# Optimization experiments

Measured on AMD Instinct MI355X. Metric: run time of the kernel, lower is better.

The kernel has to match this reference:

```python
import jax, jax.numpy as jnp
import numpy as np

BSZ, SEQLEN, D = 32, 256, 128


def setup_inputs() -> dict:
    key = jax.random.key(0)
    # Near-identity init (I + eps*N) keeps the length-256 matrix product
    # numerically stable, as in standard CMOW embeddings.
    noise = jax.random.normal(key, (BSZ, SEQLEN, D, D), dtype=jnp.float32)
    input_embeds = jnp.eye(D, dtype=jnp.float32) + 0.02 * noise
    return {"input_embeds": input_embeds}


def reference(input_embeds):
    # Cumulative (left-to-right) matrix product along the sequence axis.
    # result[:, i] = E_0 @ E_1 @ ... @ E_i  -- matmul is associative, so we
    # use a log-depth parallel scan instead of a serial per-step bmm loop.
    all_outputs = jax.lax.associative_scan(jnp.matmul, input_embeds, axis=1)
    x = all_outputs[:, -1]  # [bsz, d, d]
    return (x, all_outputs)
```

## Files before the change

### kernel.cpp

```cpp
#include <hip/hip_runtime.h>

typedef _Float16 half8_t __attribute__((ext_vector_type(8)));
typedef _Float16 half4_t __attribute__((ext_vector_type(4)));
typedef float    f32x4   __attribute__((ext_vector_type(4)));

#define BSZ 32
#define SEQ 256
#define DD  128
#define MAT 16384
#define NCH 16
#define CL  16

__device__ __forceinline__ int sw_chunk(int m, int kb) { return (m << 4) + (kb ^ (m & 7)); }
__device__ __forceinline__ int sw_off(int m, int k)    { return (sw_chunk(m, k >> 3) << 3) + (k & 7); }

__device__ __forceinline__ void mm128(const _Float16* __restrict__ Ads,
                                      const _Float16* __restrict__ Bds,
                                      f32x4 acc[4][4],
                                      int qr, int qc, int quad, int l16) {
#pragma unroll
  for (int ks = 0; ks < 4; ++ks) {
    const int kb = ks * 4 + quad;
    half8_t a[4], b[4];
#pragma unroll
    for (int tr = 0; tr < 4; ++tr)
      a[tr] = *(const half8_t*)&Ads[sw_chunk(qr * 64 + tr * 16 + l16, kb) << 3];
#pragma unroll
    for (int tc = 0; tc < 4; ++tc)
      b[tc] = *(const half8_t*)&Bds[sw_chunk(qc * 64 + tc * 16 + l16, kb) << 3];
#pragma unroll
    for (int tr = 0; tr < 4; ++tr)
#pragma unroll
      for (int tc = 0; tc < 4; ++tc)
        acc[tr][tc] = __builtin_amdgcn_mfma_f32_16x16x32_f16(a[tr], b[tc], acc[tr][tc], 0, 0, 0);
  }
}

__device__ __forceinline__ void stage_f16(const _Float16* __restrict__ src,
                                          _Float16* dst, int tid) {
#pragma unroll
  for (int it = 0; it < 8; ++it) {
    int idx = tid + it * 256;
    int m = idx >> 4, kb = idx & 15;
    *(uint4*)&dst[sw_chunk(m, kb) << 3] = ((const uint4*)src)[idx];
  }
}

__device__ __forceinline__ void acc_to_lds(_Float16* Ads, const f32x4 acc[4][4],
                                           int qr, int qc, int quad, int l16) {
#pragma unroll
  for (int tr = 0; tr < 4; ++tr)
#pragma unroll
    for (int tc = 0; tc < 4; ++tc) {
      int m0 = qr * 64 + tr * 16 + quad * 4;
      int n  = qc * 64 + tc * 16 + l16;
#pragma unroll
      for (int r = 0; r < 4; ++r) Ads[sw_off(m0 + r, n)] = (_Float16)acc[tr][tc][r];
    }
}

__device__ __forceinline__ _Float16* pT_slot(float* out_all, int b, int t) {
  return (_Float16*)(out_all + (size_t)(b * SEQ + t) * MAT) + MAT;
}

__global__ __launch_bounds__(256) void k_phase1(const float* __restrict__ in,
                                                float* __restrict__ out_all,
                                                _Float16* __restrict__ Sbuf) {
  __shared__ __align__(16) _Float16 Ads[MAT];
  __shared__ __align__(16) _Float16 Bds[MAT];
  const int tid = threadIdx.x;
  const int b = blockIdx.x >> 4, c = blockIdx.x & 15;
  const int t0 = c * CL;
  const int wave = tid >> 6, lane = tid & 63;
  const int qr = wave >> 1, qc = wave & 1, quad = lane >> 4, l16 = lane & 15;

  {
    const f32x4* src = (const f32x4*)(in + (size_t)(b * SEQ + t0) * MAT);
#pragma unroll
    for (int it = 0; it < 16; ++it) {
      int g = tid + it * 256;
      f32x4 v = src[g];
      int e0 = g << 2, m = e0 >> 7, k0 = e0 & 127;
      half4_t hv;
      hv[0] = (_Float16)v[0]; hv[1] = (_Float16)v[1];
      hv[2] = (_Float16)v[2]; hv[3] = (_Float16)v[3];
      *(half4_t*)&Ads[(sw_chunk(m, k0 >> 3) << 3) + (k0 & 7)] = hv;
    }
  }
  __syncthreads();
  {
    _Float16* dst = pT_slot(out_all, b, t0);
#pragma unroll
    for (int it = 0; it < 8; ++it) {
      int idx = tid + it * 256;
      int n = idx >> 4, m0 = (idx & 15) << 3;
      half8_t v;
#pragma unroll
      for (int j = 0; j < 8; ++j) v[j] = Ads[sw_off(m0 + j, n)];
      *(half8_t*)&dst[n * DD + m0] = v;
    }
  }

  f32x4 acc[4][4];
  for (int i = 1; i < CL; ++i) {
    {
      const f32x4* src = (const f32x4*)(in + (size_t)(b * SEQ + t0 + i) * MAT);
#pragma unroll
      for (int it = 0; it < 16; ++it) {
        int g = tid + it * 256;
        f32x4 v = src[g];
        int e0 = g << 2, k = e0 >> 7, n0 = e0 & 127;
        Bds[sw_off(n0 + 0, k)] = (_Float16)v[0];
        Bds[sw_off(n0 + 1, k)] = (_Float16)v[1];
        Bds[sw_off(n0 + 2, k)] = (_Float16)v[2];
        Bds[sw_off(n0 + 3, k)] = (_Float16)v[3];
      }
    }
    if (i > 1) acc_to_lds(Ads, acc, qr, qc, quad, l16);
    __syncthreads();
#pragma unroll
    for (int tr = 0; tr < 4; ++tr)
#pragma unroll
      for (int tc = 0; tc < 4; ++tc) { f32x4 z = {0.f, 0.f, 0.f, 0.f}; acc[tr][tc] = z; }
    mm128(Ads, Bds, acc, qr, qc, quad, l16);
    {
      _Float16* dst = pT_slot(out_all, b, t0 + i);
#pragma unroll
      for (int tr = 0; tr < 4; ++tr)
#pragma unroll
        for (int tc = 0; tc < 4; ++tc) {
          int m0 = qr * 64 + tr * 16 + quad * 4;
          int n  = qc * 64 + tc * 16 + l16;
          half4_t hv;
          hv[0] = (_Float16)acc[tr][tc][0]; hv[1] = (_Float16)acc[tr][tc][1];
          hv[2] = (_Float16)acc[tr][tc][2]; hv[3] = (_Float16)acc[tr][tc][3];
          *(half4_t*)&dst[n * DD + m0] = hv;
        }
    }
    __syncthreads();
  }

  if (c == 0) {
    acc_to_lds(Ads, acc, qr, qc, quad, l16);
    __syncthreads();
    _Float16* dst = Sbuf + (size_t)b * NCH * MAT;
#pragma unroll
    for (int it = 0; it < 8; ++it) {
      int idx = tid + it * 256;
      int m = idx >> 4, kb = idx & 15;
      *(uint4*)&dst[idx << 3] = *(const uint4*)&Ads[sw_chunk(m, kb) << 3];
    }
  }
}

__global__ __launch_bounds__(256) void k_phase2(const float* __restrict__ out_all,
                                                _Float16* __restrict__ Sbuf,
                                                float* __restrict__ out_x) {
  __shared__ __align__(16) _Float16 Ads[MAT];
  __shared__ __align__(16) _Float16 Bds[MAT];
  const int tid = threadIdx.x, b = blockIdx.x;
  const int wave = tid >> 6, lane = tid & 63;
  const int qr = wave >> 1, qc = wave & 1, quad = lane >> 4, l16 = lane & 15;

  stage_f16(Sbuf + (size_t)b * NCH * MAT, Ads, tid);

  f32x4 acc[4][4];
  for (int cc = 1; cc < NCH; ++cc) {
    stage_f16((const _Float16*)(out_all + (size_t)(b * SEQ + cc * CL + CL - 1) * MAT) + MAT,
              Bds, tid);
    __syncthreads();
#pragma unroll
    for (int tr = 0; tr < 4; ++tr)
#pragma unroll
      for (int tc = 0; tc < 4; ++tc) { f32x4 z = {0.f, 0.f, 0.f, 0.f}; acc[tr][tc] = z; }
    mm128(Ads, Bds, acc, qr, qc, quad, l16);
    __syncthreads();
    if (cc < NCH - 1) {
      acc_to_lds(Ads, acc, qr, qc, quad, l16);
      __syncthreads();
      _Float16* dst = Sbuf + ((size_t)b * NCH + cc) * MAT;
#pragma unroll
      for (int it = 0; it < 8; ++it) {
        int idx = tid + it * 256;
        int m = idx >> 4, kb = idx & 15;
        *(uint4*)&dst[idx << 3] = *(const uint4*)&Ads[sw_chunk(m, kb) << 3];
      }
    } else {
      float* xo = out_x + (size_t)b * MAT;
#pragma unroll
      for (int tr = 0; tr < 4; ++tr)
#pragma unroll
        for (int tc = 0; tc < 4; ++tc) {
          int m0 = qr * 64 + tr * 16 + quad * 4;
          int n  = qc * 64 + tc * 16 + l16;
#pragma unroll
          for (int r = 0; r < 4; ++r) xo[(m0 + r) * DD + n] = acc[tr][tc][r];
        }
    }
  }
}

__global__ __launch_bounds__(256) void k_phase3(float* __restrict__ out_all,
                                                const _Float16* __restrict__ Sbuf) {
  __shared__ __align__(16) _Float16 Ads[MAT];
  __shared__ __align__(16) _Float16 Bds[MAT];
  const int tid = threadIdx.x;
  const int b = blockIdx.x >> 4, c = blockIdx.x & 15;
  const int wave = tid >> 6, lane = tid & 63;
  const int qr = wave >> 1, qc = wave & 1, quad = lane >> 4, l16 = lane & 15;

  if (c == 0) {
    uint4 z; z.x = z.y = z.z = z.w = 0u;
#pragma unroll
    for (int it = 0; it < 8; ++it) *(uint4*)&Ads[(tid + it * 256) << 3] = z;
    __syncthreads();
    if (tid < DD) Ads[sw_off(tid, tid)] = (_Float16)1.0f;
  } else {
    stage_f16(Sbuf + ((size_t)b * NCH + (c - 1)) * MAT, Ads, tid);
  }

  f32x4 acc[4][4];
  for (int i = 0; i < CL; ++i) {
    const int t = c * CL + i;
    float* slot = out_all + (size_t)(b * SEQ + t) * MAT;
    stage_f16((const _Float16*)slot + MAT, Bds, tid);
    __syncthreads();
#pragma unroll
    for (int tr = 0; tr < 4; ++tr)
#pragma unroll
      for (int tc = 0; tc < 4; ++tc) { f32x4 z = {0.f, 0.f, 0.f, 0.f}; acc[tr][tc] = z; }
    mm128(Ads, Bds, acc, qr, qc, quad, l16);
#pragma unroll
    for (int tr = 0; tr < 4; ++tr)
#pragma unroll
      for (int tc = 0; tc < 4; ++tc) {
        int m0 = qr * 64 + tr * 16 + quad * 4;
        int n  = qc * 64 + tc * 16 + l16;
#pragma unroll
        for (int r = 0; r < 4; ++r) slot[(m0 + r) * DD + n] = acc[tr][tc][r];
      }
    __syncthreads();
  }
}

extern "C" void kernel_launch(void* const* d_in, const int* in_sizes, int n_in,
                              void* d_out, int out_size, void* d_ws, size_t ws_size,
                              hipStream_t stream) {
  const float* in = (const float*)d_in[0];
  float* out_x   = (float*)d_out;
  float* out_all = out_x + (size_t)BSZ * MAT;
  _Float16* Sbuf = (_Float16*)d_ws;

  k_phase1<<<dim3(BSZ * NCH), dim3(256), 0, stream>>>(in, out_all, Sbuf);
  k_phase2<<<dim3(BSZ), dim3(256), 0, stream>>>((const float*)out_all, Sbuf, out_x);
  k_phase3<<<dim3(BSZ * NCH), dim3(256), 0, stream>>>(out_all, Sbuf);
}
```

Before: 1.234 ms.

## Reverse operand roles to compute transposed products with prefetched register staging

The three phases now build transposed products (new matrix times the running product held in LDS), so the running accumulator can be written straight back into the B buffer and no longer needs an LDS transpose or a separate Sbuf copy pass. The next step's global data is loaded into registers while the current step computes, and lighter barriers replace __syncthreads. The fp32 outputs are now written as vector stores in transposed order, and launch bounds request two blocks per CU. In exchange, register pressure is higher, and correctness depends on the reversed-operand transposition being consistent across all three phases.

```diff
diff --git a/kernel.cpp b/kernel.cpp
--- a/kernel.cpp
+++ b/kernel.cpp
@@ -14,6 +14,17 @@
 __device__ __forceinline__ int sw_chunk(int m, int kb) { return (m << 4) + (kb ^ (m & 7)); }
 __device__ __forceinline__ int sw_off(int m, int k)    { return (sw_chunk(m, k >> 3) << 3) + (k & 7); }
 
+__device__ __forceinline__ void barrier_lgkm() {
+  asm volatile("s_waitcnt lgkmcnt(0)" ::: "memory");
+  __builtin_amdgcn_s_barrier();
+  asm volatile("" ::: "memory");
+}
+__device__ __forceinline__ void barrier_only() {
+  asm volatile("" ::: "memory");
+  __builtin_amdgcn_s_barrier();
+  asm volatile("" ::: "memory");
+}
+
 __device__ __forceinline__ void mm128(const _Float16* __restrict__ Ads,
                                       const _Float16* __restrict__ Bds,
                                       f32x4 acc[4][4],
@@ -36,36 +47,102 @@
   }
 }
 
-__device__ __forceinline__ void stage_f16(const _Float16* __restrict__ src,
-                                          _Float16* dst, int tid) {
-#pragma unroll
-  for (int it = 0; it < 8; ++it) {
-    int idx = tid + it * 256;
-    int m = idx >> 4, kb = idx & 15;
-    *(uint4*)&dst[sw_chunk(m, kb) << 3] = ((const uint4*)src)[idx];
-  }
-}
-
-__device__ __forceinline__ void acc_to_lds(_Float16* Ads, const f32x4 acc[4][4],
-                                           int qr, int qc, int quad, int l16) {
+__device__ __forceinline__ void tl_f32(const float* __restrict__ src, f32x4 ra[16],
+                                       int colg, int rowg0) {
+#pragma unroll
+  for (int p = 0; p < 4; ++p)
+#pragma unroll
+    for (int j = 0; j < 4; ++j)
+      ra[p * 4 + j] = *(const f32x4*)&src[(((rowg0 + p * 8) << 2) + j) * DD + (colg << 2)];
+}
+__device__ __forceinline__ void tw_f32(_Float16* Ads, const f32x4 ra[16],
+                                       int colg, int rowg0) {
+#pragma unroll
+  for (int p = 0; p < 4; ++p) {
+    const int k0 = (rowg0 + p * 8) << 2;
+    const int kb = k0 >> 3, kpar = k0 & 7;
+#pragma unroll
+    for (int jj = 0; jj < 4; ++jj) {
+      const int n = (colg << 2) + jj;
+      half4_t hv;
+      hv[0] = (_Float16)ra[p * 4 + 0][jj];
+      hv[1] = (_Float16)ra[p * 4 + 1][jj];
+      hv[2] = (_Float16)ra[p * 4 + 2][jj];
+      hv[3] = (_Float16)ra[p * 4 + 3][jj];
+      *(half4_t*)&Ads[(sw_chunk(n, kb) << 3) + kpar] = hv;
+    }
+  }
+}
+
+__device__ __forceinline__ void tl_f16(const _Float16* __restrict__ src, half8_t rp[8],
+                                       int colg, int rowg) {
+#pragma unroll
+  for (int h = 0; h < 2; ++h)
+#pragma unroll
+    for (int j = 0; j < 4; ++j)
+      rp[h * 4 + j] = *(const half8_t*)&src[(((rowg + h * 16) << 2) + j) * DD + (colg << 3)];
+}
+__device__ __forceinline__ void tw_f16(_Float16* Ads, const half8_t rp[8],
+                                       int colg, int rowg) {
+#pragma unroll
+  for (int h = 0; h < 2; ++h) {
+    const int k0 = (rowg + h * 16) << 2;
+    const int kb = k0 >> 3, kpar = k0 & 7;
+#pragma unroll
+    for (int jj = 0; jj < 8; ++jj) {
+      const int n = (colg << 3) + jj;
+      half4_t hv;
+      hv[0] = rp[h * 4 + 0][jj]; hv[1] = rp[h * 4 + 1][jj];
+      hv[2] = rp[h * 4 + 2][jj]; hv[3] = rp[h * 4 + 3][jj];
+      *(half4_t*)&Ads[(sw_chunk(n, kb) << 3) + kpar] = hv;
+    }
+  }
+}
+
+__device__ __forceinline__ void acc_store_f16(_Float16* __restrict__ dst,
+                                              const f32x4 acc[4][4],
+                                              int qr, int qc, int quad, int l16) {
 #pragma unroll
   for (int tr = 0; tr < 4; ++tr)
 #pragma unroll
     for (int tc = 0; tc < 4; ++tc) {
       int m0 = qr * 64 + tr * 16 + quad * 4;
       int n  = qc * 64 + tc * 16 + l16;
-#pragma unroll
-      for (int r = 0; r < 4; ++r) Ads[sw_off(m0 + r, n)] = (_Float16)acc[tr][tc][r];
-    }
-}
-
-__device__ __forceinline__ _Float16* pT_slot(float* out_all, int b, int t) {
+      half4_t hv;
+      hv[0] = (_Float16)acc[tr][tc][0]; hv[1] = (_Float16)acc[tr][tc][1];
+      hv[2] = (_Float16)acc[tr][tc][2]; hv[3] = (_Float16)acc[tr][tc][3];
+      *(half4_t*)&dst[n * DD + m0] = hv;
+    }
+}
+__device__ __forceinline__ void acc_to_bds(_Float16* Bds, const f32x4 acc[4][4],
+                                           int qr, int qc, int quad, int l16) {
+#pragma unroll
+  for (int tr = 0; tr < 4; ++tr)
+#pragma unroll
+    for (int tc = 0; tc < 4; ++tc) {
+      int m0 = qr * 64 + tr * 16 + quad * 4;
+      int n  = qc * 64 + tc * 16 + l16;
+      half4_t hv;
+      hv[0] = (_Float16)acc[tr][tc][0]; hv[1] = (_Float16)acc[tr][tc][1];
+      hv[2] = (_Float16)acc[tr][tc][2]; hv[3] = (_Float16)acc[tr][tc][3];
+      *(half4_t*)&Bds[(sw_chunk(n, m0 >> 3) << 3) + (m0 & 7)] = hv;
+    }
+}
+
+#define ZERO_ACC(acc)                                             \
+  _Pragma("unroll") for (int tr = 0; tr < 4; ++tr)                \
+  _Pragma("unroll") for (int tc = 0; tc < 4; ++tc) {              \
+    f32x4 z = {0.f, 0.f, 0.f, 0.f}; acc[tr][tc] = z; }
+
+__device__ __forceinline__ _Float16* p_slot(float* out_all, int b, int t) {
   return (_Float16*)(out_all + (size_t)(b * SEQ + t) * MAT) + MAT;
 }
-
-__global__ __launch_bounds__(256) void k_phase1(const float* __restrict__ in,
-                                                float* __restrict__ out_all,
-                                                _Float16* __restrict__ Sbuf) {
+__device__ __forceinline__ const _Float16* p_slot_c(const float* out_all, int b, int t) {
+  return (const _Float16*)(out_all + (size_t)(b * SEQ + t) * MAT) + MAT;
+}
+
+__global__ __launch_bounds__(256, 2) void k_phase1(const float* __restrict__ in,
+                                                   float* __restrict__ out_all) {
   __shared__ __align__(16) _Float16 Ads[MAT];
   __shared__ __align__(16) _Float16 Bds[MAT];
   const int tid = threadIdx.x;
@@ -73,118 +150,74 @@
   const int t0 = c * CL;
   const int wave = tid >> 6, lane = tid & 63;
   const int qr = wave >> 1, qc = wave & 1, quad = lane >> 4, l16 = lane & 15;
-
-  {
-    const f32x4* src = (const f32x4*)(in + (size_t)(b * SEQ + t0) * MAT);
+  const int colg = tid & 31, rowg0 = tid >> 5;
+
+  const float* base = in + (size_t)(b * SEQ + t0) * MAT;
+
+  f32x4 rb[16];
+  { const f32x4* s0 = (const f32x4*)base;
+#pragma unroll
+    for (int it = 0; it < 16; ++it) rb[it] = s0[tid + it * 256]; }
+  f32x4 ra[16];
+  tl_f32(base + MAT, ra, colg, rowg0);
+
+  { _Float16* g0 = p_slot(out_all, b, t0);
 #pragma unroll
     for (int it = 0; it < 16; ++it) {
-      int g = tid + it * 256;
-      f32x4 v = src[g];
-      int e0 = g << 2, m = e0 >> 7, k0 = e0 & 127;
-      half4_t hv;
-      hv[0] = (_Float16)v[0]; hv[1] = (_Float16)v[1];
-      hv[2] = (_Float16)v[2]; hv[3] = (_Float16)v[3];
-      *(half4_t*)&Ads[(sw_chunk(m, k0 >> 3) << 3) + (k0 & 7)] = hv;
-    }
-  }
-  __syncthreads();
-  {
-    _Float16* dst = pT_slot(out_all, b, t0);
-#pragma unroll
-    for (int it = 0; it < 8; ++it) {
-      int idx = tid + it * 256;
-      int n = idx >> 4, m0 = (idx & 15) << 3;
-      half8_t v;
-#pragma unroll
-      for (int j = 0; j < 8; ++j) v[j] = Ads[sw_off(m0 + j, n)];
-      *(half8_t*)&dst[n * DD + m0] = v;
-    }
-  }
+      int e0 = (tid + it * 256) << 2;
+      int m = e0 >> 7, k0 = e0 & 127;
+      half4_t hv;
+      hv[0] = (_Float16)rb[it][0]; hv[1] = (_Float16)rb[it][1];
+      hv[2] = (_Float16)rb[it][2]; hv[3] = (_Float16)rb[it][3];
+      *(half4_t*)&Bds[(sw_chunk(m, k0 >> 3) << 3) + (k0 & 7)] = hv;
+      *(half4_t*)&g0[e0] = hv;
+    } }
 
   f32x4 acc[4][4];
   for (int i = 1; i < CL; ++i) {
-    {
-      const f32x4* src = (const f32x4*)(in + (size_t)(b * SEQ + t0 + i) * MAT);
-#pragma unroll
-      for (int it = 0; it < 16; ++it) {
-        int g = tid + it * 256;
-        f32x4 v = src[g];
-        int e0 = g << 2, k = e0 >> 7, n0 = e0 & 127;
-        Bds[sw_off(n0 + 0, k)] = (_Float16)v[0];
-        Bds[sw_off(n0 + 1, k)] = (_Float16)v[1];
-        Bds[sw_off(n0 + 2, k)] = (_Float16)v[2];
-        Bds[sw_off(n0 + 3, k)] = (_Float16)v[3];
-      }
-    }
-    if (i > 1) acc_to_lds(Ads, acc, qr, qc, quad, l16);
-    __syncthreads();
-#pragma unroll
-    for (int tr = 0; tr < 4; ++tr)
-#pragma unroll
-      for (int tc = 0; tc < 4; ++tc) { f32x4 z = {0.f, 0.f, 0.f, 0.f}; acc[tr][tc] = z; }
+    tw_f32(Ads, ra, colg, rowg0);
+    if (i < CL - 1) tl_f32(base + (size_t)(i + 1) * MAT, ra, colg, rowg0);
+    barrier_lgkm();
+    ZERO_ACC(acc);
     mm128(Ads, Bds, acc, qr, qc, quad, l16);
-    {
-      _Float16* dst = pT_slot(out_all, b, t0 + i);
-#pragma unroll
-      for (int tr = 0; tr < 4; ++tr)
-#pragma unroll
-        for (int tc = 0; tc < 4; ++tc) {
-          int m0 = qr * 64 + tr * 16 + quad * 4;
-          int n  = qc * 64 + tc * 16 + l16;
-          half4_t hv;
-          hv[0] = (_Float16)acc[tr][tc][0]; hv[1] = (_Float16)acc[tr][tc][1];
-          hv[2] = (_Float16)acc[tr][tc][2]; hv[3] = (_Float16)acc[tr][tc][3];
-          *(half4_t*)&dst[n * DD + m0] = hv;
-        }
-    }
-    __syncthreads();
-  }
-
-  if (c == 0) {
-    acc_to_lds(Ads, acc, qr, qc, quad, l16);
-    __syncthreads();
-    _Float16* dst = Sbuf + (size_t)b * NCH * MAT;
-#pragma unroll
-    for (int it = 0; it < 8; ++it) {
-      int idx = tid + it * 256;
-      int m = idx >> 4, kb = idx & 15;
-      *(uint4*)&dst[idx << 3] = *(const uint4*)&Ads[sw_chunk(m, kb) << 3];
-    }
-  }
-}
-
-__global__ __launch_bounds__(256) void k_phase2(const float* __restrict__ out_all,
-                                                _Float16* __restrict__ Sbuf,
-                                                float* __restrict__ out_x) {
+    acc_store_f16(p_slot(out_all, b, t0 + i), acc, qr, qc, quad, l16);
+    barrier_only();
+    if (i < CL - 1) acc_to_bds(Bds, acc, qr, qc, quad, l16);
+  }
+}
+
+__global__ __launch_bounds__(256, 2) void k_phase2(const float* __restrict__ out_all,
+                                                   _Float16* __restrict__ Sbuf,
+                                                   float* __restrict__ out_x) {
   __shared__ __align__(16) _Float16 Ads[MAT];
   __shared__ __align__(16) _Float16 Bds[MAT];
   const int tid = threadIdx.x, b = blockIdx.x;
   const int wave = tid >> 6, lane = tid & 63;
   const int qr = wave >> 1, qc = wave & 1, quad = lane >> 4, l16 = lane & 15;
-
-  stage_f16(Sbuf + (size_t)b * NCH * MAT, Ads, tid);
+  const int colg = tid & 15, rowg = tid >> 4;
+
+  { const uint4* s = (const uint4*)p_slot_c(out_all, b, CL - 1);
+    uint4* sb0 = (uint4*)(Sbuf + (size_t)b * NCH * MAT);
+#pragma unroll
+    for (int it = 0; it < 8; ++it) {
+      int idx = tid + it * 256;
+      uint4 v = s[idx];
+      *(uint4*)&Bds[sw_chunk(idx >> 4, idx & 15) << 3] = v;
+      sb0[idx] = v;
+    } }
+  half8_t rp[8];
+  tl_f16(p_slot_c(out_all, b, 2 * CL - 1), rp, colg, rowg);
 
   f32x4 acc[4][4];
   for (int cc = 1; cc < NCH; ++cc) {
-    stage_f16((const _Float16*)(out_all + (size_t)(b * SEQ + cc * CL + CL - 1) * MAT) + MAT,
-              Bds, tid);
-    __syncthreads();
-#pragma unroll
-    for (int tr = 0; tr < 4; ++tr)
-#pragma unroll
-      for (int tc = 0; tc < 4; ++tc) { f32x4 z = {0.f, 0.f, 0.f, 0.f}; acc[tr][tc] = z; }
+    tw_f16(Ads, rp, colg, rowg);
+    if (cc < NCH - 1)
+      tl_f16(p_slot_c(out_all, b, (cc + 2) * CL - 1), rp, colg, rowg);
+    barrier_lgkm();
+    ZERO_ACC(acc);
     mm128(Ads, Bds, acc, qr, qc, quad, l16);
-    __syncthreads();
     if (cc < NCH - 1) {
-      acc_to_lds(Ads, acc, qr, qc, quad, l16);
-      __syncthreads();
-      _Float16* dst = Sbuf + ((size_t)b * NCH + cc) * MAT;
-#pragma unroll
-      for (int it = 0; it < 8; ++it) {
-        int idx = tid + it * 256;
-        int m = idx >> 4, kb = idx & 15;
-        *(uint4*)&dst[idx << 3] = *(const uint4*)&Ads[sw_chunk(m, kb) << 3];
-      }
+      acc_store_f16(Sbuf + ((size_t)b * NCH + cc) * MAT, acc, qr, qc, quad, l16);
     } else {
       float* xo = out_x + (size_t)b * MAT;
 #pragma unroll
@@ -193,53 +226,61 @@
         for (int tc = 0; tc < 4; ++tc) {
           int m0 = qr * 64 + tr * 16 + quad * 4;
           int n  = qc * 64 + tc * 16 + l16;
-#pragma unroll
-          for (int r = 0; r < 4; ++r) xo[(m0 + r) * DD + n] = acc[tr][tc][r];
+          *(f32x4*)&xo[n * DD + m0] = acc[tr][tc];
         }
     }
-  }
-}
-
-__global__ __launch_bounds__(256) void k_phase3(float* __restrict__ out_all,
-                                                const _Float16* __restrict__ Sbuf) {
+    barrier_only();
+    if (cc < NCH - 1) acc_to_bds(Bds, acc, qr, qc, quad, l16);
+  }
+}
+
+__global__ __launch_bounds__(256, 2) void k_phase3(float* __restrict__ out_all,
+                                                   const _Float16* __restrict__ Sbuf) {
   __shared__ __align__(16) _Float16 Ads[MAT];
   __shared__ __align__(16) _Float16 Bds[MAT];
   const int tid = threadIdx.x;
   const int b = blockIdx.x >> 4, c = blockIdx.x & 15;
+  const int t0 = c * CL;
   const int wave = tid >> 6, lane = tid & 63;
   const int qr = wave >> 1, qc = wave & 1, quad = lane >> 4, l16 = lane & 15;
+  const int colg = tid & 15, rowg = tid >> 4;
 
   if (c == 0) {
     uint4 z; z.x = z.y = z.z = z.w = 0u;
 #pragma unroll
-    for (int it = 0; it < 8; ++it) *(uint4*)&Ads[(tid + it * 256) << 3] = z;
-    __syncthreads();
-    if (tid < DD) Ads[sw_off(tid, tid)] = (_Float16)1.0f;
+    for (int it = 0; it < 8; ++it) *(uint4*)&Bds[(tid + it * 256) << 3] = z;
+    barrier_lgkm();
+    if (tid < DD) Bds[sw_off(tid, tid)] = (_Float16)1.0f;
   } else {
-    stage_f16(Sbuf + ((size_t)b * NCH + (c - 1)) * MAT, Ads, tid);
-  }
+    const uint4* s = (const uint4*)(Sbuf + ((size_t)b * NCH + (c - 1)) * MAT);
+#pragma unroll
+    for (int it = 0; it < 8; ++it) {
+      int idx = tid + it * 256;
+      *(uint4*)&Bds[sw_chunk(idx >> 4, idx & 15) << 3] = s[idx];
+    }
+  }
+  half8_t rp[8];
+  tl_f16(p_slot_c(out_all, b, t0), rp, colg, rowg);
 
   f32x4 acc[4][4];
   for (int i = 0; i < CL; ++i) {
-    const int t = c * CL + i;
+    const int t = t0 + i;
+    tw_f16(Ads, rp, colg, rowg);
+    if (i < CL - 1)
+      tl_f16(p_slot_c(out_all, b, t + 1), rp, colg, rowg);
+    barrier_lgkm();
+    ZERO_ACC(acc);
+    mm128(Ads, Bds, acc, qr, qc, quad, l16);
     float* slot = out_all + (size_t)(b * SEQ + t) * MAT;
-    stage_f16((const _Float16*)slot + MAT, Bds, tid);
-    __syncthreads();
-#pragma unroll
-    for (int tr = 0; tr < 4; ++tr)
-#pragma unroll
-      for (int tc = 0; tc < 4; ++tc) { f32x4 z = {0.f, 0.f, 0.f, 0.f}; acc[tr][tc] = z; }
-    mm128(Ads, Bds, acc, qr, qc, quad, l16);
 #pragma unroll
     for (int tr = 0; tr < 4; ++tr)
 #pragma unroll
       for (int tc = 0; tc < 4; ++tc) {
         int m0 = qr * 64 + tr * 16 + quad * 4;
         int n  = qc * 64 + tc * 16 + l16;
-#pragma unroll
-        for (int r = 0; r < 4; ++r) slot[(m0 + r) * DD + n] = acc[tr][tc][r];
+        *(f32x4*)&slot[n * DD + m0] = acc[tr][tc];
       }
-    __syncthreads();
+    barrier_only();
   }
 }
 
@@ -251,7 +292,7 @@
   float* out_all = out_x + (size_t)BSZ * MAT;
   _Float16* Sbuf = (_Float16*)d_ws;
 
-  k_phase1<<<dim3(BSZ * NCH), dim3(256), 0, stream>>>(in, out_all, Sbuf);
+  k_phase1<<<dim3(BSZ * NCH), dim3(256), 0, stream>>>(in, out_all);
   k_phase2<<<dim3(BSZ), dim3(256), 0, stream>>>((const float*)out_all, Sbuf, out_x);
   k_phase3<<<dim3(BSZ * NCH), dim3(256), 0, stream>>>(out_all, Sbuf);
 }
```

After: 1.044 ms. -15.4%, faster.
